# Performance work log

Hardware: AMD Instinct MI355X
Metric: run time of the kernel (lower is better)

## Reference

```python
import jax, jax.numpy as jnp
import numpy as np

N_NODES = 50000
N_EDGES = 400000
F_IN = 128
HEADS = 4
C1 = 64
C2 = 16
OUT_DIM = 2
N_GRAPHS = 64
NEG_SLOPE = 0.2


def setup_inputs() -> dict:
    key = jax.random.key(0)
    ks = jax.random.split(key, 16)
    s = 0.05
    x = jax.random.normal(ks[0], (N_NODES, F_IN), jnp.float32)
    edge_index = jax.random.randint(ks[1], (27, N_EDGES), 0, N_NODES, dtype=jnp.int32)
    batch = jnp.sort(jax.random.randint(ks[2], (N_NODES,), 0, N_GRAPHS, dtype=jnp.int32))
    return {
        "x": x,
        "edge_index": edge_index,
        "batch": batch,
        "W1": jax.random.normal(ks[3], (F_IN, HEADS * C1), jnp.float32) * s,
        "a_src1": jax.random.normal(ks[4], (HEADS, C1), jnp.float32) * s,
        "a_dst1": jax.random.normal(ks[5], (HEADS, C1), jnp.float32) * s,
        "b1": jnp.zeros((HEADS * C1,), jnp.float32),
        "W2": jax.random.normal(ks[6], (HEADS * C1, HEADS * C2), jnp.float32) * s,
        "a_src2": jax.random.normal(ks[7], (HEADS, C2), jnp.float32) * s,
        "a_dst2": jax.random.normal(ks[8], (HEADS, C2), jnp.float32) * s,
        "b2": jnp.zeros((HEADS * C2,), jnp.float32),
        "Wfc": jax.random.normal(ks[9], (HEADS * C2, OUT_DIM), jnp.float32) * s,
        "bfc": jnp.zeros((OUT_DIM,), jnp.float32),
    }


def gat_layer(x, src, dst, W, a_src, a_dst, b, out_ch):
    """PyG GATConv (concat=True, add_self_loops=True, negative_slope=0.2)."""
    n = x.shape[0]
    h = (x @ W).reshape(n, HEADS, out_ch)            # [N,H,C]
    # add self-loops (PyG default)
    loop = jnp.arange(n, dtype=src.dtype)
    src = jnp.concatenate([src, loop])
    dst = jnp.concatenate([dst, loop])
    alpha_s = jnp.einsum("nhc,hc->nh", h, a_src)      # [N,H]
    alpha_d = jnp.einsum("nhc,hc->nh", h, a_dst)
    e = jax.nn.leaky_relu(alpha_s[src] + alpha_d[dst], NEG_SLOPE)  # [E,H]
    # segment softmax over incoming edges per destination node
    m = jax.ops.segment_max(e, dst, num_segments=n)
    exp_e = jnp.exp(e - m[dst])
    denom = jax.ops.segment_sum(exp_e, dst, num_segments=n)
    alpha = exp_e / (denom[dst] + 1e-16)              # [E,H]
    out = jax.ops.segment_sum(alpha[:, :, None] * h[src], dst, num_segments=n)
    return out.reshape(n, HEADS * out_ch) + b


def reference(x, edge_index, batch, W1, a_src1, a_dst1, b1, W2, a_src2, a_dst2, b2, Wfc, bfc):
    # conv1 uses rows [17, 26] as (src, dst)
    h = gat_layer(x, edge_index[17], edge_index[26], W1, a_src1, a_dst1, b1, C1)
    h = jax.nn.relu(h)
    # conv2 uses rows [15,16,17,24,25,26]; message passing reads rows 0,1 -> (15,16)
    h = gat_layer(h, edge_index[15], edge_index[16], W2, a_src2, a_dst2, b2, C2)
    h = jax.nn.relu(h)
    # global mean pool over graphs
    sums = jax.ops.segment_sum(h, batch, num_segments=N_GRAPHS)
    cnts = jax.ops.segment_sum(jnp.ones((h.shape[0], 1), h.dtype), batch, num_segments=N_GRAPHS)
    pooled = sums / jnp.maximum(cnts, 1.0)
    return pooled @ Wfc + bfc
```

## Files before the change

### kernel.cpp

```cpp
#include <hip/hip_runtime.h>
#include <math.h>

#define HEADS 4
#define NEG_SLOPE 0.2f
#define CAP 32

static constexpr size_t OFF_H1B  = 0;
static constexpr size_t OFF_H2B  = 0;
static constexpr size_t OFF_OUT2 = 6400000;
static constexpr size_t OFF_XHI  = 25600000;
static constexpr size_t OFF_XLO  = 38400000;
static constexpr size_t OFF_O1HI = 25600000;
static constexpr size_t OFF_W1TH = 76800000;
static constexpr size_t OFF_W1TL = 76865536;
static constexpr size_t OFF_W2TH = 76931072;
static constexpr size_t OFF_W2TL = 76963840;
static constexpr size_t OFF_AS   = 77000000;
static constexpr size_t OFF_AD   = 77800000;
static constexpr size_t OFF_CNT  = 78600064;
static constexpr size_t OFF_CSR  = 79000128;

typedef __attribute__((ext_vector_type(8))) short short8;
typedef __attribute__((ext_vector_type(4))) float f32x4;

__device__ __forceinline__ float4 f4add(float4 a, float4 b) {
    return make_float4(a.x + b.x, a.y + b.y, a.z + b.z, a.w + b.w);
}
__device__ __forceinline__ float lrelu(float x) { return x > 0.f ? x : NEG_SLOPE * x; }
__device__ __forceinline__ float4 f4lrelu(float4 a) {
    return make_float4(lrelu(a.x), lrelu(a.y), lrelu(a.z), lrelu(a.w));
}
__device__ __forceinline__ float4 f4exp(float4 a) {
    return make_float4(__expf(a.x), __expf(a.y), __expf(a.z), __expf(a.w));
}
__device__ __forceinline__ float pickh(float4 v, int head) {
    float r = v.x;
    r = head == 1 ? v.y : r;
    r = head == 2 ? v.z : r;
    r = head == 3 ? v.w : r;
    return r;
}
__device__ __forceinline__ unsigned short bfr(float x) {
    union { float f; unsigned u; } c; c.f = x;
    unsigned r = c.u + 0x7FFFu + ((c.u >> 16) & 1u);
    return (unsigned short)(r >> 16);
}
__device__ __forceinline__ float bf2f(unsigned short h) {
    union { unsigned u; float f; } c; c.u = ((unsigned)h) << 16;
    return c.f;
}
__device__ __forceinline__ float2 bfpair(unsigned u) {
    union { unsigned a; float f; } lo, hi;
    lo.a = u << 16;
    hi.a = u & 0xffff0000u;
    return make_float2(lo.f, hi.f);
}

__global__ void prep_kernel(const float* __restrict__ x, unsigned short* __restrict__ xhi,
                            unsigned short* __restrict__ xlo, int n4,
                            const float* __restrict__ W1, unsigned short* __restrict__ w1th,
                            unsigned short* __restrict__ w1tl,
                            const float* __restrict__ W2, unsigned short* __restrict__ w2th,
                            unsigned short* __restrict__ w2tl,
                            int* __restrict__ cnt, int n2)
{
    const int b = blockIdx.x, t = threadIdx.x;
    if (b < 1024) {
        for (int i = b * 256 + t; i < n4; i += 1024 * 256) {
            float4 v = ((const float4*)x)[i];
            unsigned short h0 = bfr(v.x), h1 = bfr(v.y), h2 = bfr(v.z), h3 = bfr(v.w);
            unsigned short l0 = bfr(v.x - bf2f(h0)), l1 = bfr(v.y - bf2f(h1));
            unsigned short l2 = bfr(v.z - bf2f(h2)), l3 = bfr(v.w - bf2f(h3));
            ((uint2*)xhi)[i] = make_uint2((unsigned)h0 | ((unsigned)h1 << 16),
                                          (unsigned)h2 | ((unsigned)h3 << 16));
            ((uint2*)xlo)[i] = make_uint2((unsigned)l0 | ((unsigned)l1 << 16),
                                          (unsigned)l2 | ((unsigned)l3 << 16));
        }
    } else if (b < 1024 + 128) {
        int idx = (b - 1024) * 256 + t;
        const int K = 128, Nc = 256;
        int k = idx / Nc, n = idx - k * Nc;
        float v = W1[idx];
        unsigned short h = bfr(v);
        w1th[(size_t)n * K + k] = h;
        w1tl[(size_t)n * K + k] = bfr(v - bf2f(h));
    } else if (b < 1024 + 128 + 64) {
        int idx = (b - 1152) * 256 + t;
        const int K = 256, Nc = 64;
        int k = idx / Nc, n = idx - k * Nc;
        float v = W2[idx];
        unsigned short h = bfr(v);
        w2th[(size_t)n * K + k] = h;
        w2tl[(size_t)n * K + k] = bfr(v - bf2f(h));
    } else {
        int idx = (b - 1216) * 256 + t;
        if (idx < (n2 >> 2)) ((int4*)cnt)[idx] = make_int4(0, 0, 0, 0);
    }
}

__global__ __launch_bounds__(256, 2)
void gemm1_bucket_kernel(const unsigned short* __restrict__ Ahi, const unsigned short* __restrict__ Alo,
                         const unsigned short* __restrict__ BThi, const unsigned short* __restrict__ BTlo,
                         unsigned short* __restrict__ Cb,
                         const float* __restrict__ avec_s, const float* __restrict__ avec_d,
                         float* __restrict__ alpha_s, float* __restrict__ alpha_d,
                         int M, int N, int GX, int NCHUNK,
                         const int* __restrict__ src1, const int* __restrict__ dst1,
                         const int* __restrict__ src2, const int* __restrict__ dst2,
                         int* __restrict__ cnt, int* __restrict__ csr, int NN, int E)
{
    constexpr int BM = 64, BN = 128, KDIM = 128, WC = 2, CPH = 64;
    constexpr int BK    = 32;
    constexpr int WROWS = 32;
    constexpr int WCOLS = 64;
    constexpr int FR    = 2;
    constexpr int FC    = 4;
    constexpr int AP    = 1;
    constexpr int BP    = 2;

    __shared__ short As_hi[BM * BK], As_lo[BM * BK];
    __shared__ short Bs_hi[BN * BK], Bs_lo[BN * BK];

    const int group = blockIdx.x / 24;
    const int off   = blockIdx.x % 24;
    const int GEMM_CNT = GX * 2;

    if (off >= 8) {
        const int part  = blockIdx.x & 7;
        const int chunk = group * 2 + (off >= 16);
        if (chunk >= NCHUNK) return;
        const int base = chunk * 2048 + threadIdx.x;
#pragma unroll
        for (int k = 0; k < 8; ++k) {
            int e = base + k * 256;
            if (e < E) {
                int d = dst1[e];
                if ((d & 7) == part) {
                    int p = atomicAdd(&cnt[d], 1);
                    if (p < CAP) csr[(size_t)d * CAP + p] = src1[e];
                }
            } else if (e < 2 * E) {
                int d = dst2[e - E];
                if ((d & 7) == part) {
                    int p = atomicAdd(&cnt[NN + d], 1);
                    if (p < CAP) csr[((size_t)NN + d) * CAP + p] = src2[e - E];
                }
            }
        }
        return;
    }

    const int gid = group * 8 + off;
    if (gid >= GEMM_CNT) return;
    const int bx = gid % GX, by = gid / GX;
    const int tid  = threadIdx.x;
    const int w    = tid >> 6, lane = tid & 63;
    const int wr   = w / WC, wc = w % WC;
    const int lrow = lane & 15, lk = lane >> 4;
    const int m0   = bx * BM, n0 = by * BN;

    f32x4 acc[FR][FC];
#pragma unroll
    for (int i = 0; i < FR; ++i)
#pragma unroll
        for (int j = 0; j < FC; ++j) acc[i][j] = (f32x4){0.f, 0.f, 0.f, 0.f};

    short8 rAh[AP], rAl[AP], rBh[BP], rBl[BP];

    auto LOAD = [&](int kb) {
#pragma unroll
        for (int p = 0; p < AP; ++p) {
            int id = p * 256 + tid;
            int r = id >> 2, c = id & 3;
            int row = m0 + r; row = row < M ? row : M - 1;
            size_t offb = (size_t)row * KDIM + kb + c * 8;
            rAh[p] = *(const short8*)(Ahi + offb);
            rAl[p] = *(const short8*)(Alo + offb);
        }
#pragma unroll
        for (int p = 0; p < BP; ++p) {
            int id = p * 256 + tid;
            int r = id >> 2, c = id & 3;
            size_t offb = (size_t)(n0 + r) * KDIM + kb + c * 8;
            rBh[p] = *(const short8*)(BThi + offb);
            rBl[p] = *(const short8*)(BTlo + offb);
        }
    };
    auto STORE = [&]() {
#pragma unroll
        for (int p = 0; p < AP; ++p) {
            int id = p * 256 + tid;
            int r = id >> 2, c = id & 3;
            *(short8*)(&As_hi[r * BK + c * 8]) = rAh[p];
            *(short8*)(&As_lo[r * BK + c * 8]) = rAl[p];
        }
#pragma unroll
        for (int p = 0; p < BP; ++p) {
            int id = p * 256 + tid;
            int r = id >> 2, c = id & 3;
            *(short8*)(&Bs_hi[r * BK + c * 8]) = rBh[p];
            *(short8*)(&Bs_lo[r * BK + c * 8]) = rBl[p];
        }
    };

    constexpr int NT = KDIM / BK;
    LOAD(0);
    for (int t = 0; t < NT; ++t) {
        STORE();
        __syncthreads();
        if (t + 1 < NT) LOAD((t + 1) * BK);

        short8 afh[FR], afl[FR], bfh[FC], bfl[FC];
#pragma unroll
        for (int fr = 0; fr < FR; ++fr) {
            int r = wr * WROWS + fr * 16 + lrow;
            afh[fr] = *(const short8*)(&As_hi[r * BK + lk * 8]);
            afl[fr] = *(const short8*)(&As_lo[r * BK + lk * 8]);
        }
#pragma unroll
        for (int fc = 0; fc < FC; ++fc) {
            int r = wc * WCOLS + fc * 16 + lrow;
            bfh[fc] = *(const short8*)(&Bs_hi[r * BK + lk * 8]);
            bfl[fc] = *(const short8*)(&Bs_lo[r * BK + lk * 8]);
        }
#pragma unroll
        for (int fr = 0; fr < FR; ++fr)
#pragma unroll
            for (int fc = 0; fc < FC; ++fc) {
                acc[fr][fc] = __builtin_amdgcn_mfma_f32_16x16x32_bf16(afh[fr], bfh[fc], acc[fr][fc], 0, 0, 0);
                acc[fr][fc] = __builtin_amdgcn_mfma_f32_16x16x32_bf16(afh[fr], bfl[fc], acc[fr][fc], 0, 0, 0);
                acc[fr][fc] = __builtin_amdgcn_mfma_f32_16x16x32_bf16(afl[fr], bfh[fc], acc[fr][fc], 0, 0, 0);
            }
        __syncthreads();
    }

#pragma unroll
    for (int fr = 0; fr < FR; ++fr) {
        const int rbase = m0 + wr * WROWS + fr * 16 + lk * 4;
        float ps[4] = {0.f, 0.f, 0.f, 0.f}, pd[4] = {0.f, 0.f, 0.f, 0.f};
#pragma unroll
        for (int fc = 0; fc < FC; ++fc) {
            const int gc   = n0 + wc * WCOLS + fc * 16 + lrow;
            const int head = gc / CPH, ci = gc % CPH;
            const float asv = avec_s[head * CPH + ci];
            const float adv = avec_d[head * CPH + ci];
#pragma unroll
            for (int rg = 0; rg < 4; ++rg) {
                int row = rbase + rg;
                float v = acc[fr][fc][rg];
                unsigned short uh = bfr(v);
                unsigned up = (unsigned)__shfl_xor((int)(unsigned)uh, 1);
                if (!(lrow & 1) && row < M)
                    *(unsigned*)(Cb + (size_t)row * N + gc) = (unsigned)uh | (up << 16);
                ps[rg] += v * asv;
                pd[rg] += v * adv;
            }
        }
        const int head = (n0 + wc * WCOLS) / CPH;
#pragma unroll
        for (int rg = 0; rg < 4; ++rg) {
            float s = ps[rg], d = pd[rg];
#pragma unroll
            for (int m = 1; m <= 8; m <<= 1) {
                s += __shfl_xor(s, m);
                d += __shfl_xor(d, m);
            }
            if (lrow == 0 && rbase + rg < M) {
                alpha_s[(size_t)(rbase + rg) * HEADS + head] = s;
                alpha_d[(size_t)(rbase + rg) * HEADS + head] = d;
            }
        }
    }
}

template<int BM, int BN, int KDIM, int WR, int WC, int CPH, bool ALO>
__global__ __launch_bounds__(256, 2)
void mfma_gemm_gat(const unsigned short* __restrict__ Ahi, const unsigned short* __restrict__ Alo,
                   const unsigned short* __restrict__ BThi, const unsigned short* __restrict__ BTlo,
                   unsigned short* __restrict__ Cb,
                   const float* __restrict__ avec_s, const float* __restrict__ avec_d,
                   float* __restrict__ alpha_s, float* __restrict__ alpha_d,
                   int M, int N)
{
    constexpr int BK    = 32;
    constexpr int WROWS = BM / WR;
    constexpr int WCOLS = BN / WC;
    constexpr int FR    = WROWS / 16;
    constexpr int FC    = WCOLS / 16;
    constexpr int AP    = (BM * (BK / 8)) / 256;
    constexpr int BP    = (BN * (BK / 8)) / 256;
    static_assert(AP >= 1 && BP >= 1, "tile too small");

    __shared__ short As_hi[BM * BK], As_lo[ALO ? BM * BK : 64];
    __shared__ short Bs_hi[BN * BK], Bs_lo[BN * BK];

    const int tid  = threadIdx.x;
    const int w    = tid >> 6, lane = tid & 63;
    const int wr   = w / WC, wc = w % WC;
    const int lrow = lane & 15, lk = lane >> 4;
    const int m0   = blockIdx.x * BM, n0 = blockIdx.y * BN;

    f32x4 acc[FR][FC];
#pragma unroll
    for (int i = 0; i < FR; ++i)
#pragma unroll
        for (int j = 0; j < FC; ++j) acc[i][j] = (f32x4){0.f, 0.f, 0.f, 0.f};

    short8 rAh[AP], rAl[AP], rBh[BP], rBl[BP];

    auto LOAD = [&](int kb) {
#pragma unroll
        for (int p = 0; p < AP; ++p) {
            int id = p * 256 + tid;
            int r = id >> 2, c = id & 3;
            int row = m0 + r; row = row < M ? row : M - 1;
            size_t off = (size_t)row * KDIM + kb + c * 8;
            rAh[p] = *(const short8*)(Ahi + off);
            if constexpr (ALO) rAl[p] = *(const short8*)(Alo + off);
        }
#pragma unroll
        for (int p = 0; p < BP; ++p) {
            int id = p * 256 + tid;
            int r = id >> 2, c = id & 3;
            size_t off = (size_t)(n0 + r) * KDIM + kb + c * 8;
            rBh[p] = *(const short8*)(BThi + off);
            rBl[p] = *(const short8*)(BTlo + off);
        }
    };
    auto STORE = [&]() {
#pragma unroll
        for (int p = 0; p < AP; ++p) {
            int id = p * 256 + tid;
            int r = id >> 2, c = id & 3;
            *(short8*)(&As_hi[r * BK + c * 8]) = rAh[p];
            if constexpr (ALO) *(short8*)(&As_lo[r * BK + c * 8]) = rAl[p];
        }
#pragma unroll
        for (int p = 0; p < BP; ++p) {
            int id = p * 256 + tid;
            int r = id >> 2, c = id & 3;
            *(short8*)(&Bs_hi[r * BK + c * 8]) = rBh[p];
            *(short8*)(&Bs_lo[r * BK + c * 8]) = rBl[p];
        }
    };

    constexpr int NT = KDIM / BK;
    LOAD(0);
    for (int t = 0; t < NT; ++t) {
        STORE();
        __syncthreads();
        if (t + 1 < NT) LOAD((t + 1) * BK);

        short8 afh[FR], afl[FR], bfh[FC], bfl[FC];
#pragma unroll
        for (int fr = 0; fr < FR; ++fr) {
            int r = wr * WROWS + fr * 16 + lrow;
            afh[fr] = *(const short8*)(&As_hi[r * BK + lk * 8]);
            if constexpr (ALO) afl[fr] = *(const short8*)(&As_lo[r * BK + lk * 8]);
        }
#pragma unroll
        for (int fc = 0; fc < FC; ++fc) {
            int r = wc * WCOLS + fc * 16 + lrow;
            bfh[fc] = *(const short8*)(&Bs_hi[r * BK + lk * 8]);
            bfl[fc] = *(const short8*)(&Bs_lo[r * BK + lk * 8]);
        }
#pragma unroll
        for (int fr = 0; fr < FR; ++fr)
#pragma unroll
            for (int fc = 0; fc < FC; ++fc) {
                acc[fr][fc] = __builtin_amdgcn_mfma_f32_16x16x32_bf16(afh[fr], bfh[fc], acc[fr][fc], 0, 0, 0);
                acc[fr][fc] = __builtin_amdgcn_mfma_f32_16x16x32_bf16(afh[fr], bfl[fc], acc[fr][fc], 0, 0, 0);
                if constexpr (ALO)
                    acc[fr][fc] = __builtin_amdgcn_mfma_f32_16x16x32_bf16(afl[fr], bfh[fc], acc[fr][fc], 0, 0, 0);
            }
        __syncthreads();
    }

#pragma unroll
    for (int fr = 0; fr < FR; ++fr) {
        const int rbase = m0 + wr * WROWS + fr * 16 + lk * 4;
        float ps[4] = {0.f, 0.f, 0.f, 0.f}, pd[4] = {0.f, 0.f, 0.f, 0.f};
#pragma unroll
        for (int fc = 0; fc < FC; ++fc) {
            const int gc   = n0 + wc * WCOLS + fc * 16 + lrow;
            const int head = gc / CPH, ci = gc % CPH;
            const float asv = avec_s[head * CPH + ci];
            const float adv = avec_d[head * CPH + ci];
#pragma unroll
            for (int rg = 0; rg < 4; ++rg) {
                int row = rbase + rg;
                float v = acc[fr][fc][rg];
                unsigned short uh = bfr(v);
                unsigned up = (unsigned)__shfl_xor((int)(unsigned)uh, 1);
                if (!(lrow & 1) && row < M)
                    *(unsigned*)(Cb + (size_t)row * N + gc) = (unsigned)uh | (up << 16);
                ps[rg] += v * asv;
                pd[rg] += v * adv;
            }
            if constexpr (CPH == 16) {
#pragma unroll
                for (int rg = 0; rg < 4; ++rg) {
                    float s = ps[rg], d = pd[rg];
#pragma unroll
                    for (int m = 1; m <= 8; m <<= 1) {
                        s += __shfl_xor(s, m);
                        d += __shfl_xor(d, m);
                    }
                    if (lrow == 0 && rbase + rg < M) {
                        alpha_s[(size_t)(rbase + rg) * HEADS + head] = s;
                        alpha_d[(size_t)(rbase + rg) * HEADS + head] = d;
                    }
                    ps[rg] = 0.f; pd[rg] = 0.f;
                }
            }
        }
        if constexpr (CPH != 16) {
            const int head = (n0 + wc * WCOLS) / CPH;
#pragma unroll
            for (int rg = 0; rg < 4; ++rg) {
                float s = ps[rg], d = pd[rg];
#pragma unroll
                for (int m = 1; m <= 8; m <<= 1) {
                    s += __shfl_xor(s, m);
                    d += __shfl_xor(d, m);
                }
                if (lrow == 0 && rbase + rg < M) {
                    alpha_s[(size_t)(rbase + rg) * HEADS + head] = s;
                    alpha_d[(size_t)(rbase + rg) * HEADS + head] = d;
                }
            }
        }
    }
}

template<int CH, int S, bool OUTF32>
__global__ __launch_bounds__(256)
void gat_agg(const unsigned short* __restrict__ hb, const float* __restrict__ alpha_s,
             const float* __restrict__ alpha_d, const int* __restrict__ cnt,
             const int* __restrict__ csr, const float* __restrict__ bias,
             float* __restrict__ out, unsigned short* __restrict__ out_hi, int n)
{
    constexpr int CPL = CH / S;
    constexpr int NSG = 256 / S;
    static_assert(CPL == 8, "lane owns one uint4");
    __shared__ float wls[NSG][S * 5];
    const int tid    = threadIdx.x;
    const int sub    = tid / S;
    const int i      = tid % S;
    const int lane64 = tid & 63;
    const int base   = lane64 & ~(S - 1);
    const int node   = blockIdx.x * NSG + sub;
    if (node >= n) return;
    const int head = (i * CPL) / (CH / 4);
    const int deg = min(cnt[node], CAP);
    const size_t ebase = (size_t)node * CAP;

    const float4 asn = *(const float4*)(alpha_s + (size_t)node * 4);
    const float4 adn = *(const float4*)(alpha_d + (size_t)node * 4);
    float4 den = f4exp(f4lrelu(f4add(asn, adn)));
    const float wse = pickh(den, head);

    float acc[8];
    {
        uint4 hv = *(const uint4*)(hb + (size_t)node * CH + i * 8);
        float2 q0 = bfpair(hv.x), q1 = bfpair(hv.y), q2 = bfpair(hv.z), q3 = bfpair(hv.w);
        acc[0] = wse * q0.x; acc[1] = wse * q0.y; acc[2] = wse * q1.x; acc[3] = wse * q1.y;
        acc[4] = wse * q2.x; acc[5] = wse * q2.y; acc[6] = wse * q3.x; acc[7] = wse * q3.y;
    }

    for (int ch = 0; ch < deg; ch += S) {
        const int cntc = min(S, deg - ch);
        float4 w4 = make_float4(0.f, 0.f, 0.f, 0.f);
        int sl = 0;
        if (i < cntc) {
            sl = csr[ebase + ch + i];
            float4 al = *(const float4*)(alpha_s + (size_t)sl * 4);
            w4 = f4exp(f4lrelu(f4add(al, adn)));
        }
        float4 t = w4;
#pragma unroll
        for (int d = S / 2; d >= 1; d >>= 1) {
            t.x += __shfl_xor(t.x, d);
            t.y += __shfl_xor(t.y, d);
            t.z += __shfl_xor(t.z, d);
            t.w += __shfl_xor(t.w, d);
        }
        den = f4add(den, t);
        wls[sub][i * 5 + 0] = w4.x;
        wls[sub][i * 5 + 1] = w4.y;
        wls[sub][i * 5 + 2] = w4.z;
        wls[sub][i * 5 + 3] = w4.w;

        const int padded = (cntc + 7) & ~7;
        for (int j = 0; j < padded; j += 8) {
            int   sk[8];
            float wk[8];
#pragma unroll
            for (int k = 0; k < 8; ++k) {
                sk[k] = __shfl(sl, base + ((j + k) < S ? (j + k) : 0));
                wk[k] = wls[sub][(j + k) * 5 + head];
            }
            uint4 v[8];
#pragma unroll
            for (int k = 0; k < 8; ++k)
                v[k] = *(const uint4*)(hb + (size_t)sk[k] * CH + i * 8);
#pragma unroll
            for (int k = 0; k < 8; ++k) {
                float2 q0 = bfpair(v[k].x), q1 = bfpair(v[k].y);
                float2 q2 = bfpair(v[k].z), q3 = bfpair(v[k].w);
                acc[0] += wk[k] * q0.x; acc[1] += wk[k] * q0.y;
                acc[2] += wk[k] * q1.x; acc[3] += wk[k] * q1.y;
                acc[4] += wk[k] * q2.x; acc[5] += wk[k] * q2.y;
                acc[6] += wk[k] * q3.x; acc[7] += wk[k] * q3.y;
            }
        }
    }

    const float invd = 1.0f / (pickh(den, head) + 1e-16f);
    const int c0 = i * CPL;
    float o[8];
#pragma unroll
    for (int k = 0; k < 8; ++k)
        o[k] = fmaxf(acc[k] * invd + bias[c0 + k], 0.f);
    if constexpr (OUTF32) {
        *(float4*)(out + (size_t)node * CH + c0)     = make_float4(o[0], o[1], o[2], o[3]);
        *(float4*)(out + (size_t)node * CH + c0 + 4) = make_float4(o[4], o[5], o[6], o[7]);
    } else {
        unsigned short oh[8];
#pragma unroll
        for (int k = 0; k < 8; ++k) oh[k] = bfr(o[k]);
        uint4 ph;
        ph.x = (unsigned)oh[0] | ((unsigned)oh[1] << 16);
        ph.y = (unsigned)oh[2] | ((unsigned)oh[3] << 16);
        ph.z = (unsigned)oh[4] | ((unsigned)oh[5] << 16);
        ph.w = (unsigned)oh[6] | ((unsigned)oh[7] << 16);
        *(uint4*)(out_hi + (size_t)node * CH + c0) = ph;
    }
}

__global__ __launch_bounds__(256)
void pool_fc_kernel(const float* __restrict__ feat, const int* __restrict__ batch,
                    const float* __restrict__ Wfc, const float* __restrict__ bfc,
                    float* __restrict__ out, int n)
{
    __shared__ float4 part[16][16];
    __shared__ float pooled[64];
    __shared__ int sb[2];
    const int g = blockIdx.x;
    const int t = threadIdx.x;
    if (t < 2) {
        int target = g + t;
        int lo = 0, hi = n;
        while (lo < hi) {
            int mid = (lo + hi) >> 1;
            if (batch[mid] < target) lo = mid + 1; else hi = mid;
        }
        sb[t] = lo;
    }
    __syncthreads();
    const int s0 = sb[0], s1 = sb[1];
    const int q = t & 15, ns = t >> 4;
    float4 acc = make_float4(0.f, 0.f, 0.f, 0.f);
    for (int i = s0 + ns; i < s1; i += 16)
        acc = f4add(acc, *(const float4*)(feat + (size_t)i * 64 + q * 4));
    part[ns][q] = acc;
    __syncthreads();
    if (t < 16) {
        float4 s = part[0][t];
#pragma unroll
        for (int k = 1; k < 16; ++k) s = f4add(s, part[k][t]);
        float inv = 1.0f / fmaxf((float)(s1 - s0), 1.0f);
        pooled[t * 4 + 0] = s.x * inv;
        pooled[t * 4 + 1] = s.y * inv;
        pooled[t * 4 + 2] = s.z * inv;
        pooled[t * 4 + 3] = s.w * inv;
    }
    __syncthreads();
    if (t < 2) {
        float a = bfc[t];
        for (int c = 0; c < 64; ++c) a += pooled[c] * Wfc[c * 2 + t];
        out[g * 2 + t] = a;
    }
}

extern "C" void kernel_launch(void* const* d_in, const int* in_sizes, int n_in,
                              void* d_out, int out_size, void* d_ws, size_t ws_size,
                              hipStream_t stream)
{
    const float* x    = (const float*)d_in[0];
    const int*   ei   = (const int*)d_in[1];
    const int*   batch= (const int*)d_in[2];
    const float* W1   = (const float*)d_in[3];
    const float* as1  = (const float*)d_in[4];
    const float* ad1  = (const float*)d_in[5];
    const float* b1   = (const float*)d_in[6];
    const float* W2   = (const float*)d_in[7];
    const float* as2  = (const float*)d_in[8];
    const float* ad2  = (const float*)d_in[9];
    const float* b2   = (const float*)d_in[10];
    const float* Wfc  = (const float*)d_in[11];
    const float* bfc  = (const float*)d_in[12];
    float* out = (float*)d_out;

    const int N = in_sizes[2];
    const int E = in_sizes[1] / 27;
    const int F = in_sizes[0] / N;

    char* ws = (char*)d_ws;
    unsigned short* h1b   = (unsigned short*)(ws + OFF_H1B);
    unsigned short* h2b   = (unsigned short*)(ws + OFF_H2B);
    float*          out2  = (float*)(ws + OFF_OUT2);
    unsigned short* xhi   = (unsigned short*)(ws + OFF_XHI);
    unsigned short* xlo   = (unsigned short*)(ws + OFF_XLO);
    unsigned short* o1hi  = (unsigned short*)(ws + OFF_O1HI);
    unsigned short* w1th  = (unsigned short*)(ws + OFF_W1TH);
    unsigned short* w1tl  = (unsigned short*)(ws + OFF_W1TL);
    unsigned short* w2th  = (unsigned short*)(ws + OFF_W2TH);
    unsigned short* w2tl  = (unsigned short*)(ws + OFF_W2TL);
    float* al_s  = (float*)(ws + OFF_AS);
    float* al_d  = (float*)(ws + OFF_AD);
    int*   cnt   = (int*)(ws + OFF_CNT);
    int*   csr   = (int*)(ws + OFF_CSR);

    const int NCH = (2 * E + 2047) / 2048;
    const int ZB  = ((2 * N / 4) + 255) / 256;
    const int GX  = (N + 63) / 64;
    const int GROUPS = ((GX * 2 + 7) / 8 > (NCH + 1) / 2) ? (GX * 2 + 7) / 8
                                                          : (NCH + 1) / 2;

    prep_kernel<<<1216 + ZB, 256, 0, stream>>>(x, xhi, xlo, N * F / 4,
                                               W1, w1th, w1tl, W2, w2th, w2tl,
                                               cnt, 2 * N);

    gemm1_bucket_kernel<<<GROUPS * 24, 256, 0, stream>>>(
        xhi, xlo, w1th, w1tl, h1b, as1, ad1, al_s, al_d, N, HEADS * 64, GX, NCH,
        ei + 17 * (size_t)E, ei + 26 * (size_t)E,
        ei + 15 * (size_t)E, ei + 16 * (size_t)E,
        cnt, csr, N, E);

    gat_agg<256, 32, false><<<(N + 7) / 8, 256, 0, stream>>>(h1b, al_s, al_d, cnt, csr, b1,
                                                             nullptr, o1hi, N);

    {
        dim3 g((N + 63) / 64, 1);
        mfma_gemm_gat<64, 64, 256, 2, 2, 16, false><<<g, 256, 0, stream>>>(
            o1hi, nullptr, w2th, w2tl, h2b, as2, ad2, al_s, al_d, N, HEADS * 16);
    }
    gat_agg<64, 8, true><<<(N + 31) / 32, 256, 0, stream>>>(h2b, al_s, al_d, cnt + N,
                                                            csr + (size_t)N * CAP, b2,
                                                            out2, nullptr, N);

    pool_fc_kernel<<<64, 256, 0, stream>>>(out2, batch, Wfc, bfc, out, N);
}
```

Baseline: 152.0 us.

## Fuse x bf16 split into GEMM1 and move layer-2 bucketing into agg1

Drops the separate pass that split x into bf16 hi/lo arrays; GEMM1 now reads fp32 x directly and converts to hi/lo in registers while loading tiles. The layer-2 CSR bucketing is moved out of the GEMM1 kernel and into a new layer-1 aggregation kernel, which interleaves bucket blocks with aggregation blocks. This removes a full read and write of x through the workspace and balances the atomic scatter work across two kernels. The cost is extra conversion arithmetic inside the GEMM load path and a new, specialised aggregation kernel.

```diff
diff --git a/kernel.cpp b/kernel.cpp
--- a/kernel.cpp
+++ b/kernel.cpp
@@ -8,8 +8,6 @@
 static constexpr size_t OFF_H1B  = 0;
 static constexpr size_t OFF_H2B  = 0;
 static constexpr size_t OFF_OUT2 = 6400000;
-static constexpr size_t OFF_XHI  = 25600000;
-static constexpr size_t OFF_XLO  = 38400000;
 static constexpr size_t OFF_O1HI = 25600000;
 static constexpr size_t OFF_W1TH = 76800000;
 static constexpr size_t OFF_W1TL = 76865536;
@@ -56,36 +54,23 @@
     return make_float2(lo.f, hi.f);
 }
 
-__global__ void prep_kernel(const float* __restrict__ x, unsigned short* __restrict__ xhi,
-                            unsigned short* __restrict__ xlo, int n4,
-                            const float* __restrict__ W1, unsigned short* __restrict__ w1th,
+__global__ void prep_kernel(const float* __restrict__ W1, unsigned short* __restrict__ w1th,
                             unsigned short* __restrict__ w1tl,
                             const float* __restrict__ W2, unsigned short* __restrict__ w2th,
                             unsigned short* __restrict__ w2tl,
                             int* __restrict__ cnt, int n2)
 {
     const int b = blockIdx.x, t = threadIdx.x;
-    if (b < 1024) {
-        for (int i = b * 256 + t; i < n4; i += 1024 * 256) {
-            float4 v = ((const float4*)x)[i];
-            unsigned short h0 = bfr(v.x), h1 = bfr(v.y), h2 = bfr(v.z), h3 = bfr(v.w);
-            unsigned short l0 = bfr(v.x - bf2f(h0)), l1 = bfr(v.y - bf2f(h1));
-            unsigned short l2 = bfr(v.z - bf2f(h2)), l3 = bfr(v.w - bf2f(h3));
-            ((uint2*)xhi)[i] = make_uint2((unsigned)h0 | ((unsigned)h1 << 16),
-                                          (unsigned)h2 | ((unsigned)h3 << 16));
-            ((uint2*)xlo)[i] = make_uint2((unsigned)l0 | ((unsigned)l1 << 16),
-                                          (unsigned)l2 | ((unsigned)l3 << 16));
-        }
-    } else if (b < 1024 + 128) {
-        int idx = (b - 1024) * 256 + t;
+    if (b < 128) {
+        int idx = b * 256 + t;
         const int K = 128, Nc = 256;
         int k = idx / Nc, n = idx - k * Nc;
         float v = W1[idx];
         unsigned short h = bfr(v);
         w1th[(size_t)n * K + k] = h;
         w1tl[(size_t)n * K + k] = bfr(v - bf2f(h));
-    } else if (b < 1024 + 128 + 64) {
-        int idx = (b - 1152) * 256 + t;
+    } else if (b < 128 + 64) {
+        int idx = (b - 128) * 256 + t;
         const int K = 256, Nc = 64;
         int k = idx / Nc, n = idx - k * Nc;
         float v = W2[idx];
@@ -93,41 +78,35 @@
         w2th[(size_t)n * K + k] = h;
         w2tl[(size_t)n * K + k] = bfr(v - bf2f(h));
     } else {
-        int idx = (b - 1216) * 256 + t;
+        int idx = (b - 192) * 256 + t;
         if (idx < (n2 >> 2)) ((int4*)cnt)[idx] = make_int4(0, 0, 0, 0);
     }
 }
 
 __global__ __launch_bounds__(256, 2)
-void gemm1_bucket_kernel(const unsigned short* __restrict__ Ahi, const unsigned short* __restrict__ Alo,
+void gemm1_bucket_kernel(const float* __restrict__ X,
                          const unsigned short* __restrict__ BThi, const unsigned short* __restrict__ BTlo,
                          unsigned short* __restrict__ Cb,
                          const float* __restrict__ avec_s, const float* __restrict__ avec_d,
                          float* __restrict__ alpha_s, float* __restrict__ alpha_d,
                          int M, int N, int GX, int NCHUNK,
                          const int* __restrict__ src1, const int* __restrict__ dst1,
-                         const int* __restrict__ src2, const int* __restrict__ dst2,
-                         int* __restrict__ cnt, int* __restrict__ csr, int NN, int E)
+                         int* __restrict__ cnt, int* __restrict__ csr, int E)
 {
     constexpr int BM = 64, BN = 128, KDIM = 128, WC = 2, CPH = 64;
-    constexpr int BK    = 32;
-    constexpr int WROWS = 32;
-    constexpr int WCOLS = 64;
-    constexpr int FR    = 2;
-    constexpr int FC    = 4;
-    constexpr int AP    = 1;
-    constexpr int BP    = 2;
+    constexpr int BK = 32;
+    constexpr int WROWS = 32, WCOLS = 64, FR = 2, FC = 4, BP = 2;
 
     __shared__ short As_hi[BM * BK], As_lo[BM * BK];
     __shared__ short Bs_hi[BN * BK], Bs_lo[BN * BK];
 
-    const int group = blockIdx.x / 24;
-    const int off   = blockIdx.x % 24;
+    const int group = blockIdx.x / 16;
+    const int off   = blockIdx.x % 16;
     const int GEMM_CNT = GX * 2;
 
     if (off >= 8) {
         const int part  = blockIdx.x & 7;
-        const int chunk = group * 2 + (off >= 16);
+        const int chunk = group;
         if (chunk >= NCHUNK) return;
         const int base = chunk * 2048 + threadIdx.x;
 #pragma unroll
@@ -139,12 +118,6 @@
                     int p = atomicAdd(&cnt[d], 1);
                     if (p < CAP) csr[(size_t)d * CAP + p] = src1[e];
                 }
-            } else if (e < 2 * E) {
-                int d = dst2[e - E];
-                if ((d & 7) == part) {
-                    int p = atomicAdd(&cnt[NN + d], 1);
-                    if (p < CAP) csr[((size_t)NN + d) * CAP + p] = src2[e - E];
-                }
             }
         }
         return;
@@ -165,17 +138,23 @@
 #pragma unroll
         for (int j = 0; j < FC; ++j) acc[i][j] = (f32x4){0.f, 0.f, 0.f, 0.f};
 
-    short8 rAh[AP], rAl[AP], rBh[BP], rBl[BP];
+    short8 rAh, rAl;
+    short8 rBh[BP], rBl[BP];
 
     auto LOAD = [&](int kb) {
-#pragma unroll
-        for (int p = 0; p < AP; ++p) {
-            int id = p * 256 + tid;
-            int r = id >> 2, c = id & 3;
+        {
+            int r = tid >> 2, c = tid & 3;
             int row = m0 + r; row = row < M ? row : M - 1;
-            size_t offb = (size_t)row * KDIM + kb + c * 8;
-            rAh[p] = *(const short8*)(Ahi + offb);
-            rAl[p] = *(const short8*)(Alo + offb);
+            const float* xp = X + (size_t)row * KDIM + kb + c * 8;
+            float4 v0 = *(const float4*)xp;
+            float4 v1 = *(const float4*)(xp + 4);
+            float vv[8] = {v0.x, v0.y, v0.z, v0.w, v1.x, v1.y, v1.z, v1.w};
+#pragma unroll
+            for (int k = 0; k < 8; ++k) {
+                unsigned short h = bfr(vv[k]);
+                rAh[k] = (short)h;
+                rAl[k] = (short)bfr(vv[k] - bf2f(h));
+            }
         }
 #pragma unroll
         for (int p = 0; p < BP; ++p) {
@@ -187,12 +166,10 @@
         }
     };
     auto STORE = [&]() {
-#pragma unroll
-        for (int p = 0; p < AP; ++p) {
-            int id = p * 256 + tid;
-            int r = id >> 2, c = id & 3;
-            *(short8*)(&As_hi[r * BK + c * 8]) = rAh[p];
-            *(short8*)(&As_lo[r * BK + c * 8]) = rAl[p];
+        {
+            int r = tid >> 2, c = tid & 3;
+            *(short8*)(&As_hi[r * BK + c * 8]) = rAh;
+            *(short8*)(&As_lo[r * BK + c * 8]) = rAl;
         }
 #pragma unroll
         for (int p = 0; p < BP; ++p) {
@@ -271,6 +248,129 @@
             }
         }
     }
+}
+
+__global__ __launch_bounds__(256)
+void agg1_bucket_kernel(const unsigned short* __restrict__ hb, const float* __restrict__ alpha_s,
+                        const float* __restrict__ alpha_d, const int* __restrict__ cnt,
+                        const int* __restrict__ csr, const float* __restrict__ bias,
+                        unsigned short* __restrict__ out_hi, int n, int NCHUNK,
+                        const int* __restrict__ src2, const int* __restrict__ dst2,
+                        int* __restrict__ cnt2, int* __restrict__ csr2, int E)
+{
+    constexpr int CH = 256, S = 32, CPL = 8, NSG = 8;
+    __shared__ float wls[NSG][S * 5];
+
+    const int group = blockIdx.x / 40;
+    const int off   = blockIdx.x % 40;
+
+    if (off >= 32) {
+        const int part  = blockIdx.x & 7;
+        const int chunk = group;
+        if (chunk >= NCHUNK) return;
+        const int base = chunk * 2048 + threadIdx.x;
+#pragma unroll
+        for (int k = 0; k < 8; ++k) {
+            int e = base + k * 256;
+            if (e < E) {
+                int d = dst2[e];
+                if ((d & 7) == part) {
+                    int p = atomicAdd(&cnt2[d], 1);
+                    if (p < CAP) csr2[(size_t)d * CAP + p] = src2[e];
+                }
+            }
+        }
+        return;
+    }
+
+    const int gid = group * 32 + off;
+    const int tid    = threadIdx.x;
+    const int sub    = tid / S;
+    const int i      = tid % S;
+    const int lane64 = tid & 63;
+    const int base   = lane64 & ~(S - 1);
+    const int node   = gid * NSG + sub;
+    if (node >= n) return;
+    const int head = (i * CPL) / (CH / 4);
+    const int deg = min(cnt[node], CAP);
+    const size_t ebase = (size_t)node * CAP;
+
+    const float4 asn = *(const float4*)(alpha_s + (size_t)node * 4);
+    const float4 adn = *(const float4*)(alpha_d + (size_t)node * 4);
+    float4 den = f4exp(f4lrelu(f4add(asn, adn)));
+    const float wse = pickh(den, head);
+
+    float acc[8];
+    {
+        uint4 hv = *(const uint4*)(hb + (size_t)node * CH + i * 8);
+        float2 q0 = bfpair(hv.x), q1 = bfpair(hv.y), q2 = bfpair(hv.z), q3 = bfpair(hv.w);
+        acc[0] = wse * q0.x; acc[1] = wse * q0.y; acc[2] = wse * q1.x; acc[3] = wse * q1.y;
+        acc[4] = wse * q2.x; acc[5] = wse * q2.y; acc[6] = wse * q3.x; acc[7] = wse * q3.y;
+    }
+
+    for (int ch = 0; ch < deg; ch += S) {
+        const int cntc = min(S, deg - ch);
+        float4 w4 = make_float4(0.f, 0.f, 0.f, 0.f);
+        int sl = 0;
+        if (i < cntc) {
+            sl = csr[ebase + ch + i];
+            float4 al = *(const float4*)(alpha_s + (size_t)sl * 4);
+            w4 = f4exp(f4lrelu(f4add(al, adn)));
+        }
+        float4 t = w4;
+#pragma unroll
+        for (int d = S / 2; d >= 1; d >>= 1) {
+            t.x += __shfl_xor(t.x, d);
+            t.y += __shfl_xor(t.y, d);
+            t.z += __shfl_xor(t.z, d);
+            t.w += __shfl_xor(t.w, d);
+        }
+        den = f4add(den, t);
+        wls[sub][i * 5 + 0] = w4.x;
+        wls[sub][i * 5 + 1] = w4.y;
+        wls[sub][i * 5 + 2] = w4.z;
+        wls[sub][i * 5 + 3] = w4.w;
+
+        const int padded = (cntc + 7) & ~7;
+        for (int j = 0; j < padded; j += 8) {
+            int   sk[8];
+            float wk[8];
+#pragma unroll
+            for (int k = 0; k < 8; ++k) {
+                sk[k] = __shfl(sl, base + ((j + k) < S ? (j + k) : 0));
+                wk[k] = wls[sub][(j + k) * 5 + head];
+            }
+            uint4 v[8];
+#pragma unroll
+            for (int k = 0; k < 8; ++k)
+                v[k] = *(const uint4*)(hb + (size_t)sk[k] * CH + i * 8);
+#pragma unroll
+            for (int k = 0; k < 8; ++k) {
+                float2 q0 = bfpair(v[k].x), q1 = bfpair(v[k].y);
+                float2 q2 = bfpair(v[k].z), q3 = bfpair(v[k].w);
+                acc[0] += wk[k] * q0.x; acc[1] += wk[k] * q0.y;
+                acc[2] += wk[k] * q1.x; acc[3] += wk[k] * q1.y;
+                acc[4] += wk[k] * q2.x; acc[5] += wk[k] * q2.y;
+                acc[6] += wk[k] * q3.x; acc[7] += wk[k] * q3.y;
+            }
+        }
+    }
+
+    const float invd = 1.0f / (pickh(den, head) + 1e-16f);
+    const int c0 = i * CPL;
+    float o[8];
+    unsigned short oh[8];
+#pragma unroll
+    for (int k = 0; k < 8; ++k) {
+        o[k] = fmaxf(acc[k] * invd + bias[c0 + k], 0.f);
+        oh[k] = bfr(o[k]);
+    }
+    uint4 ph;
+    ph.x = (unsigned)oh[0] | ((unsigned)oh[1] << 16);
+    ph.y = (unsigned)oh[2] | ((unsigned)oh[3] << 16);
+    ph.z = (unsigned)oh[4] | ((unsigned)oh[5] << 16);
+    ph.w = (unsigned)oh[6] | ((unsigned)oh[7] << 16);
+    *(uint4*)(out_hi + (size_t)node * CH + c0) = ph;
 }
 
 template<int BM, int BN, int KDIM, int WR, int WC, int CPH, bool ALO>
@@ -610,8 +710,6 @@
     unsigned short* h1b   = (unsigned short*)(ws + OFF_H1B);
     unsigned short* h2b   = (unsigned short*)(ws + OFF_H2B);
     float*          out2  = (float*)(ws + OFF_OUT2);
-    unsigned short* xhi   = (unsigned short*)(ws + OFF_XHI);
-    unsigned short* xlo   = (unsigned short*)(ws + OFF_XLO);
     unsigned short* o1hi  = (unsigned short*)(ws + OFF_O1HI);
     unsigned short* w1th  = (unsigned short*)(ws + OFF_W1TH);
     unsigned short* w1tl  = (unsigned short*)(ws + OFF_W1TL);
@@ -622,24 +720,24 @@
     int*   cnt   = (int*)(ws + OFF_CNT);
     int*   csr   = (int*)(ws + OFF_CSR);
 
-    const int NCH = (2 * E + 2047) / 2048;
-    const int ZB  = ((2 * N / 4) + 255) / 256;
-    const int GX  = (N + 63) / 64;
-    const int GROUPS = ((GX * 2 + 7) / 8 > (NCH + 1) / 2) ? (GX * 2 + 7) / 8
-                                                          : (NCH + 1) / 2;
-
-    prep_kernel<<<1216 + ZB, 256, 0, stream>>>(x, xhi, xlo, N * F / 4,
-                                               W1, w1th, w1tl, W2, w2th, w2tl,
-                                               cnt, 2 * N);
-
-    gemm1_bucket_kernel<<<GROUPS * 24, 256, 0, stream>>>(
-        xhi, xlo, w1th, w1tl, h1b, as1, ad1, al_s, al_d, N, HEADS * 64, GX, NCH,
-        ei + 17 * (size_t)E, ei + 26 * (size_t)E,
+    const int NCH1 = (E + 2047) / 2048;
+    const int ZB   = ((2 * N / 4) + 255) / 256;
+    const int GX   = (N + 63) / 64;
+
+    const int G1 = ((GX * 2 + 7) / 8 > NCH1) ? (GX * 2 + 7) / 8 : NCH1;
+    const int AGG_BLOCKS = (N + 7) / 8;
+    const int G2 = ((AGG_BLOCKS + 31) / 32 > NCH1) ? (AGG_BLOCKS + 31) / 32 : NCH1;
+
+    prep_kernel<<<192 + ZB, 256, 0, stream>>>(W1, w1th, w1tl, W2, w2th, w2tl, cnt, 2 * N);
+
+    gemm1_bucket_kernel<<<G1 * 16, 256, 0, stream>>>(
+        x, w1th, w1tl, h1b, as1, ad1, al_s, al_d, N, HEADS * 64, GX, NCH1,
+        ei + 17 * (size_t)E, ei + 26 * (size_t)E, cnt, csr, E);
+
+    agg1_bucket_kernel<<<G2 * 40, 256, 0, stream>>>(
+        h1b, al_s, al_d, cnt, csr, b1, o1hi, N, NCH1,
         ei + 15 * (size_t)E, ei + 16 * (size_t)E,
-        cnt, csr, N, E);
-
-    gat_agg<256, 32, false><<<(N + 7) / 8, 256, 0, stream>>>(h1b, al_s, al_d, cnt, csr, b1,
-                                                             nullptr, o1hi, N);
+        cnt + N, csr + (size_t)N * CAP, E);
 
     {
         dim3 g((N + 63) / 64, 1);
```

New measurement: 155.6 us. +2.4%, slower.
